# Kernel optimization log

Measured on AMD Instinct MI355X. Metric: run time of the kernel, lower is better.

## Reference

```python
import jax, jax.numpy as jnp
import numpy as np

B, L, H, N = 8, 4096, 1024, 32  # batch, seq_len, hidden_size, complex state modes


def setup_inputs() -> dict:
    key = jax.random.key(0)
    k0, k1, k2, k3 = jax.random.split(key, 4)
    u = jax.random.normal(k0, (B, L, H), jnp.float32)
    # S4D standard init: dt log-uniform in [1e-3, 1e-1]
    log_dt = jnp.log(0.001) + jax.random.uniform(k1, (H,), jnp.float32) * (
        jnp.log(0.1) - jnp.log(0.001))
    # A = -exp(A_real) + i*A_imag ; S4D-Lin init: Re=-0.5, Im=pi*n
    A_real = jnp.full((H, N), jnp.log(0.5), jnp.float32)
    A_imag = jnp.broadcast_to(jnp.pi * jnp.arange(N, dtype=jnp.float32), (H, N))
    C_real = jax.random.normal(k2, (H, N), jnp.float32) * (0.5 ** 0.5)
    C_imag = jax.random.normal(k3, (H, N), jnp.float32) * (0.5 ** 0.5)
    D = jnp.asarray(0.0, jnp.float32)
    return dict(u=u, log_dt=log_dt, A_real=A_real, A_imag=A_imag,
                C_real=C_real, C_imag=C_imag, D=D)


def _s4d_kernel(log_dt, A_real, A_imag, C_real, C_imag, seq_len):
    """Diagonal SSM conv kernel K of shape (H, seq_len)."""
    dt = jnp.exp(log_dt)[:, None]                      # (H, 1)
    A = -jnp.exp(A_real) + 1j * A_imag                 # (H, N)
    dtA = A * dt                                       # (H, N)
    C = (C_real + 1j * C_imag) * (jnp.exp(dtA) - 1.0) / A  # (H, N)
    # Vandermonde: exp(dtA)^l for l = 0..L-1  -> (H, N, L)
    vand = jnp.exp(dtA[:, :, None] * jnp.arange(seq_len, dtype=jnp.float32))
    return 2.0 * jnp.einsum('hn,hnl->hl', C, vand).real  # (H, L)


def reference(u, log_dt, A_real, A_imag, C_real, C_imag, D):
    seq_len = u.shape[1]
    K = _s4d_kernel(log_dt, A_real, A_imag, C_real, C_imag, seq_len)  # (H, L)
    n_fft = 2 * seq_len  # zero-pad for linear (causal) convolution
    u_f = jnp.fft.rfft(u, n=n_fft, axis=1)               # (B, L+1, H)
    k_f = jnp.fft.rfft(K, n=n_fft, axis=-1).T            # (L+1, H)
    y = jnp.fft.irfft(u_f * k_f[None], n=n_fft, axis=1)[:, :seq_len]  # (B, L, H)
    y = y + D * u
    return jax.nn.gelu(y, approximate=False)  # torch nn.GELU default = erf
```

## Files before the change

kernel.cpp:

```cpp
#include <hip/hip_runtime.h>
#include <hip/hip_bf16.h>


#define B_ 8
#define L_ 4096
#define H_ 1024
#define N_ 32
#define NH_ 16
#define NQ_ 8

__global__ void modes_kernel(const float* __restrict__ log_dt,
                             const float* __restrict__ A_real,
                             const float* __restrict__ A_imag,
                             const float* __restrict__ C_real,
                             const float* __restrict__ C_imag,
                             float4* __restrict__ modes,
                             float2* __restrict__ wLc,
                             int log2Lc) {
    int t = blockIdx.x * blockDim.x + threadIdx.x;
    if (t >= H_ * N_) return;
    int h = t / N_, n = t % N_;
    float dt = expf(log_dt[h]);
    float ar = -expf(A_real[t]);
    float ai = A_imag[t];
    float cr = C_real[t];
    float ci = C_imag[t];
    float dr = ar * dt, di = ai * dt;
    float e = expf(dr);
    float sn, cs;
    sincosf(di, &sn, &cs);
    float wr = e * cs, wi = e * sn;
    float inv = 1.0f / (ar * ar + ai * ai);
    float nr = wr - 1.0f, ni = wi;
    float qr = (nr * ar + ni * ai) * inv;
    float qi = (ni * ar - nr * ai) * inv;
    float gr = 2.0f * (cr * qr - ci * qi);
    float gi = -2.0f * (cr * qi + ci * qr);
    modes[n * H_ + h] = make_float4(wr, wi, gr, gi);
    float pr = wr, pi2 = wi;
    for (int i = 0; i < log2Lc; ++i) {
        float t2r = pr * pr - pi2 * pi2;
        float t2i = 2.0f * pr * pi2;
        pr = t2r; pi2 = t2i;
    }
    wLc[n * H_ + h] = make_float2(pr, pi2);
}

template <int C_>
__global__ __launch_bounds__(256, 8) void scan_local(const float* __restrict__ u,
                                                     const float4* __restrict__ modes,
                                                     float2* __restrict__ states) {
    constexpr int Lc = L_ / C_;
    int t = blockIdx.x * blockDim.x + threadIdx.x;
    int lane = t & 63;
    int w = t >> 6;
    int q = lane >> 4;
    int k = lane & 15;
    int h = (w & 63) * 16 + k;
    int bc = w >> 6;
    int c = bc % C_;
    int b = bc / C_;
    int nb = q * NQ_;
    float wr[NQ_], wi[NQ_], sr[NQ_], si[NQ_];
#pragma unroll
    for (int n = 0; n < NQ_; ++n) {
        float4 m = modes[(nb + n) * H_ + h];
        wr[n] = m.x; wi[n] = m.y; sr[n] = 0.0f; si[n] = 0.0f;
    }
    unsigned idx = ((unsigned)b * L_ + (unsigned)c * Lc) * H_ + (unsigned)h;
    float pre[4];
#pragma unroll
    for (int s = 0; s < 4; ++s) pre[s] = u[idx + (unsigned)(s * H_)];
    for (int j = 0; j < Lc; j += 4) {
#pragma unroll
        for (int s = 0; s < 4; ++s) {
            float uv = pre[s];
            pre[s] = u[idx + (unsigned)((((j + 4 + s) & (Lc - 1))) * H_)];
#pragma unroll
            for (int n = 0; n < NQ_; ++n) {
                float tr = fmaf(wr[n], sr[n], fmaf(-wi[n], si[n], uv));
                float ti = fmaf(wr[n], si[n], wi[n] * sr[n]);
                sr[n] = tr; si[n] = ti;
            }
        }
    }
    float2* sp = states + ((size_t)bc * N_ + nb) * H_ + h;
#pragma unroll
    for (int n = 0; n < NQ_; ++n) sp[(size_t)n * H_] = make_float2(sr[n], si[n]);
}

template <int C_>
__global__ __launch_bounds__(256) void chunk_scan(const float2* __restrict__ wLc,
                                                  float2* __restrict__ states) {
    int t = blockIdx.x * blockDim.x + threadIdx.x;
    int h = t % H_;
    int bn = t / H_;
    int n = bn % N_;
    int b = bn / N_;
    float2 wl = wLc[n * H_ + h];
    float er = 0.0f, ei = 0.0f;
    float2* p0 = states + ((size_t)(b * C_) * N_ + n) * H_ + h;
    const size_t stride = (size_t)N_ * H_;
    float2 nxt = *p0;
#pragma unroll
    for (int c = 0; c < C_; ++c) {
        float2 le = nxt;
        float2* p = p0 + (size_t)c * stride;
        if (c + 1 < C_) nxt = p[stride];
        *p = make_float2(er, ei);
        float nr2 = fmaf(wl.x, er, fmaf(-wl.y, ei, le.x));
        float ni2 = fmaf(wl.x, ei, fmaf(wl.y, er, le.y));
        er = nr2; ei = ni2;
    }
}

template <int C_>
__global__ __launch_bounds__(256, 4) void scan_out(const float* __restrict__ u,
                                                   const float4* __restrict__ modes,
                                                   const float2* __restrict__ states,
                                                   const float* __restrict__ Dscal,
                                                   float* __restrict__ y) {
    constexpr int Lc = L_ / C_;
    int t = blockIdx.x * blockDim.x + threadIdx.x;
    int lane = t & 63;
    int w = t >> 6;
    int half = lane >> 5;
    int k = lane & 31;
    int h = (w & 31) * 32 + k;
    int bc = w >> 5;
    int c = bc % C_;
    int b = bc / C_;
    int nb = half * NH_;
    float Dv = Dscal[0];
    float wr[NH_], wi[NH_], gr[NH_], gi[NH_], sr[NH_], si[NH_];
#pragma unroll
    for (int n = 0; n < NH_; ++n) {
        float4 m = modes[(nb + n) * H_ + h];
        wr[n] = m.x; wi[n] = m.y; gr[n] = m.z; gi[n] = m.w;
        float2 e = states[((size_t)bc * N_ + nb + n) * H_ + h];
        sr[n] = e.x; si[n] = e.y;
    }
    unsigned idx = ((unsigned)b * L_ + (unsigned)c * Lc) * H_ + (unsigned)h;
    unsigned idy = idx + (unsigned)(half * H_);
    float pre0 = u[idx];
    float pre1 = u[idx + (unsigned)H_];
    for (int j = 0; j < Lc; j += 2) {
        float uvA = pre0, uvB = pre1;
        pre0 = u[idx + (unsigned)(((j + 2) & (Lc - 1)) * H_)];
        pre1 = u[idx + (unsigned)(((j + 3) & (Lc - 1)) * H_)];
        float accA = 0.0f, accB = 0.0f;
#pragma unroll
        for (int n = 0; n < NH_; ++n) {
            float tr = fmaf(wr[n], sr[n], fmaf(-wi[n], si[n], uvA));
            float ti = fmaf(wr[n], si[n], wi[n] * sr[n]);
            accA = fmaf(gr[n], tr, fmaf(gi[n], ti, accA));
            float tr2 = fmaf(wr[n], tr, fmaf(-wi[n], ti, uvB));
            float ti2 = fmaf(wr[n], ti, wi[n] * tr);
            sr[n] = tr2; si[n] = ti2;
            accB = fmaf(gr[n], tr2, fmaf(gi[n], ti2, accB));
        }
        accA += __shfl_xor(accA, 32, 64);
        accB += __shfl_xor(accB, 32, 64);
        float uvS = half ? uvB : uvA;
        float accS = half ? accB : accA;
        float v = fmaf(Dv, uvS, accS);
        float g = 0.5f * v * (1.0f + erff(v * 0.70710678118654752f));
        y[idy + (unsigned)(j * H_)] = g;
    }
}

template <int C_>
static void launch_all(const float* u, const float* log_dt, const float* A_real,
                       const float* A_imag, const float* C_real, const float* C_imag,
                       const float* Dscal, float* y, char* ws, hipStream_t stream) {
    float4* modes = (float4*)ws;
    float2* wLc   = (float2*)(ws + 524288);
    float2* states = (float2*)(ws + 786432);
    int log2Lc = 0;
    for (int v = L_ / C_; v > 1; v >>= 1) ++log2Lc;

    constexpr int nwaves_local = B_ * C_ * (H_ / 16);
    constexpr int nblocks_local = nwaves_local / 4;
    constexpr int nwaves_out = B_ * C_ * (H_ / 32);
    constexpr int nblocks_out = nwaves_out / 4;

    modes_kernel<<<(H_ * N_) / 256, 256, 0, stream>>>(log_dt, A_real, A_imag,
                                                      C_real, C_imag, modes, wLc, log2Lc);
    scan_local<C_><<<nblocks_local, 256, 0, stream>>>(u, modes, states);
    chunk_scan<C_><<<(B_ * N_ * H_) / 256, 256, 0, stream>>>(wLc, states);
    scan_out<C_><<<nblocks_out, 256, 0, stream>>>(u, modes, states, Dscal, y);
}

extern "C" void kernel_launch(void* const* d_in, const int* in_sizes, int n_in,
                              void* d_out, int out_size, void* d_ws, size_t ws_size,
                              hipStream_t stream) {
    const float* u      = (const float*)d_in[0];
    const float* log_dt = (const float*)d_in[1];
    const float* A_real = (const float*)d_in[2];
    const float* A_imag = (const float*)d_in[3];
    const float* C_real = (const float*)d_in[4];
    const float* C_imag = (const float*)d_in[5];
    const float* Dscal  = (const float*)d_in[6];
    float* y = (float*)d_out;
    char* ws = (char*)d_ws;

    const size_t base = 786432;
    auto need = [&](int C) { return base + (size_t)B_ * C * N_ * H_ * 8; };
    if (ws_size >= need(32)) {
        launch_all<32>(u, log_dt, A_real, A_imag, C_real, C_imag, Dscal, y, ws, stream);
    } else if (ws_size >= need(16)) {
        launch_all<16>(u, log_dt, A_real, A_imag, C_real, C_imag, Dscal, y, ws, stream);
    } else {
        launch_all<8>(u, log_dt, A_real, A_imag, C_real, C_imag, Dscal, y, ws, stream);
    }
}
```

Baseline: 481.3 us.

## Split scan_out modes across four lane quarters with butterfly reduction and 4-step unroll

scan_out now assigns 8 modes per lane quarter instead of 16 per half-wave. Each thread advances four timesteps per body and combines the quarter partial sums with a two-stage shuffle butterfly, so each lane writes one output per four steps. This quarters the per-lane output and GELU work and halves register state, allowing a waves_per_eu hint of 6. scan_local gets the same double-buffered 4x unrolled prefetch pattern without the modulo wraparound loads. The cost is more shuffles and selects per step, and the same u values are loaded redundantly by each quarter.

```diff
diff --git a/kernel.cpp b/kernel.cpp
--- a/kernel.cpp
+++ b/kernel.cpp
@@ -1,12 +1,10 @@
 #include <hip/hip_runtime.h>
-#include <hip/hip_bf16.h>
 
 
 #define B_ 8
 #define L_ 4096
 #define H_ 1024
 #define N_ 32
-#define NH_ 16
 #define NQ_ 8
 
 __global__ void modes_kernel(const float* __restrict__ log_dt,
@@ -46,6 +44,27 @@
     wLc[n * H_ + h] = make_float2(pr, pi2);
 }
 
+
+#define SLOC_BODY(U0, U1, U2, U3, DO_PF) do {                                   \
+    _Pragma("unroll")                                                           \
+    for (int n = 0; n < NQ_; ++n) {                                             \
+        float t1r = fmaf(wr[n], sr[n], fmaf(-wi[n], si[n], (U0)));              \
+        float t1i = fmaf(wr[n], si[n], wi[n] * sr[n]);                          \
+        float t2r = fmaf(wr[n], t1r, fmaf(-wi[n], t1i, (U1)));                  \
+        float t2i = fmaf(wr[n], t1i, wi[n] * t1r);                              \
+        float t3r = fmaf(wr[n], t2r, fmaf(-wi[n], t2i, (U2)));                  \
+        float t3i = fmaf(wr[n], t2i, wi[n] * t2r);                              \
+        float t4r = fmaf(wr[n], t3r, fmaf(-wi[n], t3i, (U3)));                  \
+        float t4i = fmaf(wr[n], t3i, wi[n] * t3r);                              \
+        sr[n] = t4r; si[n] = t4i;                                               \
+    }                                                                           \
+    if (DO_PF) {                                                                \
+        (U0) = u[pf]; (U1) = u[pf + H_]; (U2) = u[pf + 2u * H_];                \
+        (U3) = u[pf + 3u * H_];                                                 \
+        pf += 4u * H_;                                                          \
+    }                                                                           \
+} while (0)
+
 template <int C_>
 __global__ __launch_bounds__(256, 8) void scan_local(const float* __restrict__ u,
                                                      const float4* __restrict__ modes,
@@ -58,8 +77,6 @@
     int k = lane & 15;
     int h = (w & 63) * 16 + k;
     int bc = w >> 6;
-    int c = bc % C_;
-    int b = bc / C_;
     int nb = q * NQ_;
     float wr[NQ_], wi[NQ_], sr[NQ_], si[NQ_];
 #pragma unroll
@@ -67,23 +84,22 @@
         float4 m = modes[(nb + n) * H_ + h];
         wr[n] = m.x; wi[n] = m.y; sr[n] = 0.0f; si[n] = 0.0f;
     }
-    unsigned idx = ((unsigned)b * L_ + (unsigned)c * Lc) * H_ + (unsigned)h;
-    float pre[4];
-#pragma unroll
-    for (int s = 0; s < 4; ++s) pre[s] = u[idx + (unsigned)(s * H_)];
-    for (int j = 0; j < Lc; j += 4) {
-#pragma unroll
-        for (int s = 0; s < 4; ++s) {
-            float uv = pre[s];
-            pre[s] = u[idx + (unsigned)((((j + 4 + s) & (Lc - 1))) * H_)];
-#pragma unroll
-            for (int n = 0; n < NQ_; ++n) {
-                float tr = fmaf(wr[n], sr[n], fmaf(-wi[n], si[n], uv));
-                float ti = fmaf(wr[n], si[n], wi[n] * sr[n]);
-                sr[n] = tr; si[n] = ti;
-            }
-        }
-    }
+    unsigned idx = (unsigned)bc * (unsigned)(Lc * H_) + (unsigned)h;
+    float a0 = u[idx];
+    float a1 = u[idx + H_];
+    float a2 = u[idx + 2u * H_];
+    float a3 = u[idx + 3u * H_];
+    float b0 = u[idx + 4u * H_];
+    float b1 = u[idx + 5u * H_];
+    float b2 = u[idx + 6u * H_];
+    float b3 = u[idx + 7u * H_];
+    unsigned pf = idx + 8u * H_;
+    for (int j = 0; j + 8 < Lc; j += 8) {
+        SLOC_BODY(a0, a1, a2, a3, 1);
+        SLOC_BODY(b0, b1, b2, b3, 1);
+    }
+    SLOC_BODY(a0, a1, a2, a3, 0);
+    SLOC_BODY(b0, b1, b2, b3, 0);
     float2* sp = states + ((size_t)bc * N_ + nb) * H_ + h;
 #pragma unroll
     for (int n = 0; n < NQ_; ++n) sp[(size_t)n * H_] = make_float2(sr[n], si[n]);
@@ -114,59 +130,93 @@
     }
 }
 
-template <int C_>
-__global__ __launch_bounds__(256, 4) void scan_out(const float* __restrict__ u,
-                                                   const float4* __restrict__ modes,
-                                                   const float2* __restrict__ states,
-                                                   const float* __restrict__ Dscal,
-                                                   float* __restrict__ y) {
+#define SOUT_BODY(U0, U1, U2, U3, DO_PF) do {                                   \
+    float accA = 0.0f, accB = 0.0f, accC = 0.0f, accD = 0.0f;                   \
+    _Pragma("unroll")                                                           \
+    for (int n = 0; n < NQ_; ++n) {                                             \
+        float t1r = fmaf(wr[n], sr[n], fmaf(-wi[n], si[n], (U0)));              \
+        float t1i = fmaf(wr[n], si[n], wi[n] * sr[n]);                          \
+        accA = fmaf(gr[n], t1r, fmaf(gi[n], t1i, accA));                        \
+        float t2r = fmaf(wr[n], t1r, fmaf(-wi[n], t1i, (U1)));                  \
+        float t2i = fmaf(wr[n], t1i, wi[n] * t1r);                              \
+        accB = fmaf(gr[n], t2r, fmaf(gi[n], t2i, accB));                        \
+        float t3r = fmaf(wr[n], t2r, fmaf(-wi[n], t2i, (U2)));                  \
+        float t3i = fmaf(wr[n], t2i, wi[n] * t2r);                              \
+        accC = fmaf(gr[n], t3r, fmaf(gi[n], t3i, accC));                        \
+        float t4r = fmaf(wr[n], t3r, fmaf(-wi[n], t3i, (U3)));                  \
+        float t4i = fmaf(wr[n], t3i, wi[n] * t3r);                              \
+        accD = fmaf(gr[n], t4r, fmaf(gi[n], t4i, accD));                        \
+        sr[n] = t4r; si[n] = t4i;                                               \
+    }                                                                           \
+          \
+    float r0 = hiq ? accC : accA;                                               \
+    float r1 = hiq ? accA : accC;                                               \
+    float p0 = r0 + __shfl_xor(r1, 32, 64);                                     \
+    float r2 = hiq ? accD : accB;                                               \
+    float r3 = hiq ? accB : accD;                                               \
+    float p1 = r2 + __shfl_xor(r3, 32, 64);                                     \
+             \
+    float snd = oddq ? p0 : p1;                                                 \
+    float bse = oddq ? p1 : p0;                                                 \
+    float accS = bse + __shfl_xor(snd, 16, 64);                                 \
+    float uv01 = oddq ? (U1) : (U0);                                            \
+    float uv23 = oddq ? (U3) : (U2);                                            \
+    float uvS = hiq ? uv23 : uv01;                                              \
+    float v = fmaf(Dv, uvS, accS);                                              \
+    float g = 0.5f * v * (1.0f + erff(v * 0.70710678118654752f));               \
+    y[sy] = g;                                                                  \
+    sy += 4u * H_;                                                              \
+    if (DO_PF) {                                                                \
+        (U0) = u[pf]; (U1) = u[pf + H_]; (U2) = u[pf + 2u * H_];                \
+        (U3) = u[pf + 3u * H_];                                                 \
+        pf += 4u * H_;                                                          \
+    }                                                                           \
+} while (0)
+
+template <int C_>
+__global__ __launch_bounds__(256) __attribute__((amdgpu_waves_per_eu(6, 6)))
+void scan_out(const float* __restrict__ u,
+              const float4* __restrict__ modes,
+              const float2* __restrict__ states,
+              const float* __restrict__ Dscal,
+              float* __restrict__ y) {
     constexpr int Lc = L_ / C_;
     int t = blockIdx.x * blockDim.x + threadIdx.x;
     int lane = t & 63;
     int w = t >> 6;
-    int half = lane >> 5;
-    int k = lane & 31;
-    int h = (w & 31) * 32 + k;
-    int bc = w >> 5;
-    int c = bc % C_;
-    int b = bc / C_;
-    int nb = half * NH_;
+    int q = lane >> 4;
+    int k = lane & 15;
+    int h = (w & 63) * 16 + k;
+    int bc = w >> 6;
+    int nb = q * NQ_;
+    bool hiq = (lane & 32) != 0;
+    bool oddq = (lane & 16) != 0;
     float Dv = Dscal[0];
-    float wr[NH_], wi[NH_], gr[NH_], gi[NH_], sr[NH_], si[NH_];
-#pragma unroll
-    for (int n = 0; n < NH_; ++n) {
+    float wr[NQ_], wi[NQ_], gr[NQ_], gi[NQ_], sr[NQ_], si[NQ_];
+#pragma unroll
+    for (int n = 0; n < NQ_; ++n) {
         float4 m = modes[(nb + n) * H_ + h];
         wr[n] = m.x; wi[n] = m.y; gr[n] = m.z; gi[n] = m.w;
         float2 e = states[((size_t)bc * N_ + nb + n) * H_ + h];
         sr[n] = e.x; si[n] = e.y;
     }
-    unsigned idx = ((unsigned)b * L_ + (unsigned)c * Lc) * H_ + (unsigned)h;
-    unsigned idy = idx + (unsigned)(half * H_);
-    float pre0 = u[idx];
-    float pre1 = u[idx + (unsigned)H_];
-    for (int j = 0; j < Lc; j += 2) {
-        float uvA = pre0, uvB = pre1;
-        pre0 = u[idx + (unsigned)(((j + 2) & (Lc - 1)) * H_)];
-        pre1 = u[idx + (unsigned)(((j + 3) & (Lc - 1)) * H_)];
-        float accA = 0.0f, accB = 0.0f;
-#pragma unroll
-        for (int n = 0; n < NH_; ++n) {
-            float tr = fmaf(wr[n], sr[n], fmaf(-wi[n], si[n], uvA));
-            float ti = fmaf(wr[n], si[n], wi[n] * sr[n]);
-            accA = fmaf(gr[n], tr, fmaf(gi[n], ti, accA));
-            float tr2 = fmaf(wr[n], tr, fmaf(-wi[n], ti, uvB));
-            float ti2 = fmaf(wr[n], ti, wi[n] * tr);
-            sr[n] = tr2; si[n] = ti2;
-            accB = fmaf(gr[n], tr2, fmaf(gi[n], ti2, accB));
-        }
-        accA += __shfl_xor(accA, 32, 64);
-        accB += __shfl_xor(accB, 32, 64);
-        float uvS = half ? uvB : uvA;
-        float accS = half ? accB : accA;
-        float v = fmaf(Dv, uvS, accS);
-        float g = 0.5f * v * (1.0f + erff(v * 0.70710678118654752f));
-        y[idy + (unsigned)(j * H_)] = g;
-    }
+    unsigned idx = (unsigned)bc * (unsigned)(Lc * H_) + (unsigned)h;
+    unsigned sy = idx + (unsigned)(q * H_);
+    float a0 = u[idx];
+    float a1 = u[idx + H_];
+    float a2 = u[idx + 2u * H_];
+    float a3 = u[idx + 3u * H_];
+    float b0 = u[idx + 4u * H_];
+    float b1 = u[idx + 5u * H_];
+    float b2 = u[idx + 6u * H_];
+    float b3 = u[idx + 7u * H_];
+    unsigned pf = idx + 8u * H_;
+    for (int j = 0; j + 8 < Lc; j += 8) {
+        SOUT_BODY(a0, a1, a2, a3, 1);
+        SOUT_BODY(b0, b1, b2, b3, 1);
+    }
+    SOUT_BODY(a0, a1, a2, a3, 0);
+    SOUT_BODY(b0, b1, b2, b3, 0);
 }
 
 template <int C_>
@@ -179,16 +229,14 @@
     int log2Lc = 0;
     for (int v = L_ / C_; v > 1; v >>= 1) ++log2Lc;
 
-    constexpr int nwaves_local = B_ * C_ * (H_ / 16);
-    constexpr int nblocks_local = nwaves_local / 4;
-    constexpr int nwaves_out = B_ * C_ * (H_ / 32);
-    constexpr int nblocks_out = nwaves_out / 4;
+    constexpr int nwaves = B_ * C_ * (H_ / 16);
+    constexpr int nblocks = nwaves / 4;
 
     modes_kernel<<<(H_ * N_) / 256, 256, 0, stream>>>(log_dt, A_real, A_imag,
                                                       C_real, C_imag, modes, wLc, log2Lc);
-    scan_local<C_><<<nblocks_local, 256, 0, stream>>>(u, modes, states);
+    scan_local<C_><<<nblocks, 256, 0, stream>>>(u, modes, states);
     chunk_scan<C_><<<(B_ * N_ * H_) / 256, 256, 0, stream>>>(wLc, states);
-    scan_out<C_><<<nblocks_out, 256, 0, stream>>>(u, modes, states, Dscal, y);
+    scan_out<C_><<<nblocks, 256, 0, stream>>>(u, modes, states, Dscal, y);
 }
 
 extern "C" void kernel_launch(void* const* d_in, const int* in_sizes, int n_in,
```

After: 1.007 ms. 2.09x slower.
